# Optimization experiments

Measured on AMD Instinct MI355X. Metric: run time of the kernel, lower is better.

## Reference

```python
import jax, jax.numpy as jnp
import numpy as np

N, E = 50000, 800000
IN_D, HID_D, OUT_D = 128, 64, 64
EPS_BN = 1e-5
NEG_SLOPE = 0.2


def _xavier(key, shape):
    fan_in, fan_out = shape[0], shape[-1]
    lim = float(np.sqrt(6.0 / (fan_in + fan_out)))
    return jax.random.uniform(key, shape, jnp.float32, -lim, lim)


def setup_inputs() -> dict:
    key = jax.random.key(0)
    ks = jax.random.split(key, 10)
    x = jax.random.normal(ks[0], (N, IN_D), jnp.float32)
    edge_index = jax.random.randint(ks[1], (2, E), 0, N, jnp.int64)
    return {
        "x": x,
        "edge_index": edge_index,
        "W1": _xavier(ks[2], (IN_D, HID_D)),
        "att_src1": _xavier(ks[3], (1, HID_D))[0],
        "att_dst1": _xavier(ks[4], (1, HID_D))[0],
        "bias1": jnp.zeros((HID_D,), jnp.float32),
        "gamma": jnp.ones((HID_D,), jnp.float32),
        "beta": jnp.zeros((HID_D,), jnp.float32),
        "W2": _xavier(ks[5], (HID_D, OUT_D)),
        "att_src2": _xavier(ks[6], (1, OUT_D))[0],
        "att_dst2": _xavier(ks[7], (1, OUT_D))[0],
        "bias2": jnp.zeros((OUT_D,), jnp.float32),
    }


def _gat_conv(x, src, dst, W, a_src, a_dst, bias, n_nodes):
    # h: [N, D_out]; messages flow src -> dst; softmax over edges per dst node
    h = x @ W
    alpha_s = h @ a_src  # [N]
    alpha_d = h @ a_dst  # [N]
    e = jax.nn.leaky_relu(alpha_s[src] + alpha_d[dst], NEG_SLOPE)  # [E]
    e_max = jax.ops.segment_max(e, dst, num_segments=n_nodes)
    e = jnp.exp(e - e_max[dst])
    denom = jax.ops.segment_sum(e, dst, num_segments=n_nodes)
    alpha = e / (denom[dst] + 1e-16)  # [E]
    out = jax.ops.segment_sum(h[src] * alpha[:, None], dst, num_segments=n_nodes)
    return out + bias


def _batchnorm(x, gamma, beta):
    mu = jnp.mean(x, axis=0)
    var = jnp.var(x, axis=0)
    return (x - mu) * jax.lax.rsqrt(var + EPS_BN) * gamma + beta


def reference(x, edge_index, W1, att_src1, att_dst1, bias1, gamma, beta,
              W2, att_src2, att_dst2, bias2):
    n_nodes = x.shape[0]
    loops = jnp.arange(n_nodes, dtype=edge_index.dtype)
    src = jnp.concatenate([edge_index[0], loops])  # add self loops (PyG default)
    dst = jnp.concatenate([edge_index[1], loops])
    h = _gat_conv(x, src, dst, W1, att_src1, att_dst1, bias1, n_nodes)
    h = jax.nn.relu(_batchnorm(h, gamma, beta))
    return _gat_conv(h, src, dst, W2, att_src2, att_dst2, bias2, n_nodes)
```

## Files before the change

### kernel.cpp

```cpp
#include <hip/hip_runtime.h>

#define N_NODES 50000
#define E_EDGES 800000
#define NE_TOT  (E_EDGES + N_NODES)
#define IND     128
#define HID     64
#define CAP_X   32
#define NEG_SLOPE 0.2f

typedef short v8s __attribute__((ext_vector_type(8)));
typedef float v4f __attribute__((ext_vector_type(4)));

#define SWZ(row, byte) ((byte) ^ (((row) & 7) << 4))

static __device__ __forceinline__ unsigned short f2bf(float f) {
    unsigned u = __float_as_uint(f);
    return (unsigned short)((u + 0x7FFF + ((u >> 16) & 1)) >> 16);
}
static __device__ __forceinline__ float bf2f(unsigned short u) {
    return __uint_as_float(((unsigned)u) << 16);
}

__global__ void k_init(const float* __restrict__ W1, const float* __restrict__ W2,
                       int* __restrict__ cnt, float* __restrict__ sums,
                       unsigned short* __restrict__ w1t, unsigned short* __restrict__ w2t) {
    int g = blockIdx.x * 256 + threadIdx.x;
    if (g < 8 * N_NODES) cnt[g] = 0;
    if (g < 128) sums[g] = 0.f;
    if (g < 64 * IND) { int c = g >> 7, k = g & 127; w1t[g] = f2bf(W1[k * 64 + c]); }
    if (g < 64 * 64)  { int c = g >> 6, k = g & 63;  w2t[g] = f2bf(W2[k * 64 + c]); }
}

__global__ void k_scatter(const int* __restrict__ ei, int* __restrict__ cnt,
                          unsigned short* __restrict__ bucket) {
    int xcc;
    asm("s_getreg_b32 %0, hwreg(20, 0, 32)" : "=s"(xcc));
    xcc &= 7;
    int e = blockIdx.x * 256 + threadIdx.x;
    if (e >= NE_TOT) return;
    int s, d;
    if (e < E_EDGES) { s = ei[e]; d = ei[E_EDGES + e]; }
    else { s = d = e - E_EDGES; }
    int pos = atomicAdd(&cnt[xcc * N_NODES + d], 1);
    if (pos < CAP_X) bucket[((size_t)(xcc * CAP_X + pos)) * N_NODES + d] = (unsigned short)s;
}

__global__ __launch_bounds__(256) void k_gemm1(
    const float* __restrict__ x, const unsigned short* __restrict__ w1t,
    const float* __restrict__ as_w, const float* __restrict__ ad_w,
    unsigned short* __restrict__ hbf, float* __restrict__ as_out, float* __restrict__ ad_out)
{
    __shared__ __align__(16) char sA[64 * 256];
    __shared__ __align__(16) char sB[64 * 256];
    __shared__ float sAs[64], sAd[64];
    int tid = threadIdx.x;
    int row0 = blockIdx.x * 64;

#pragma unroll
    for (int i = 0; i < 8; ++i) {
        int idx = i * 256 + tid;
        int r = idx >> 5, c4 = idx & 31;
        int gr = row0 + r; if (gr >= N_NODES) gr = N_NODES - 1;
        float4 v = ((const float4*)(x + (size_t)gr * IND))[c4];
        ushort4 b; b.x = f2bf(v.x); b.y = f2bf(v.y); b.z = f2bf(v.z); b.w = f2bf(v.w);
        *(ushort4*)(sA + r * 256 + SWZ(r, c4 * 8)) = b;
    }
#pragma unroll
    for (int i = 0; i < 4; ++i) {
        int idx = i * 256 + tid;
        int r = idx >> 4, c8 = idx & 15;
        v8s wv = *(const v8s*)(w1t + idx * 8);
        *(v8s*)(sB + r * 256 + SWZ(r, c8 * 16)) = wv;
    }
    if (tid < 64) { sAs[tid] = as_w[tid]; sAd[tid] = ad_w[tid]; }
    __syncthreads();

    int w = tid >> 6, lane = tid & 63;
    int arow = w * 16 + (lane & 15);
    int kb   = (lane >> 4) * 16;
    v4f acc[4] = {};
#pragma unroll
    for (int ks = 0; ks < 4; ++ks) {
        v8s a = *(const v8s*)(sA + arow * 256 + SWZ(arow, ks * 64 + kb));
#pragma unroll
        for (int ct = 0; ct < 4; ++ct) {
            int brow = ct * 16 + (lane & 15);
            v8s b = *(const v8s*)(sB + brow * 256 + SWZ(brow, ks * 64 + kb));
            acc[ct] = __builtin_amdgcn_mfma_f32_16x16x32_bf16(a, b, acc[ct], 0, 0, 0);
        }
    }

    int cbase = lane & 15;
    int rloc  = (lane >> 4) * 4;
#pragma unroll
    for (int ct = 0; ct < 4; ++ct)
#pragma unroll
        for (int rg = 0; rg < 4; ++rg) {
            int row = row0 + w * 16 + rloc + rg;
            if (row < N_NODES) hbf[(size_t)row * 64 + ct * 16 + cbase] = f2bf(acc[ct][rg]);
        }
#pragma unroll
    for (int rg = 0; rg < 4; ++rg) {
        float vs = 0.f, vd = 0.f;
#pragma unroll
        for (int ct = 0; ct < 4; ++ct) {
            vs = fmaf(acc[ct][rg], sAs[ct * 16 + cbase], vs);
            vd = fmaf(acc[ct][rg], sAd[ct * 16 + cbase], vd);
        }
        vs += __shfl_xor(vs, 1, 64); vd += __shfl_xor(vd, 1, 64);
        vs += __shfl_xor(vs, 2, 64); vd += __shfl_xor(vd, 2, 64);
        vs += __shfl_xor(vs, 4, 64); vd += __shfl_xor(vd, 4, 64);
        vs += __shfl_xor(vs, 8, 64); vd += __shfl_xor(vd, 8, 64);
        int row = row0 + w * 16 + rloc + rg;
        if (cbase == 0 && row < N_NODES) { as_out[row] = vs; ad_out[row] = vd; }
    }
}

template <bool OUT_BF16>
__global__ __launch_bounds__(256) void k_agg(
    const unsigned short* __restrict__ hin, const float* __restrict__ as_, const float* __restrict__ ad_,
    const int* __restrict__ cnt, const unsigned short* __restrict__ bucket,
    const float* __restrict__ bias, void* __restrict__ outv)
{
    int wave = threadIdx.x >> 6, lane = threadIdx.x & 63;
    int n = blockIdx.x * 4 + wave;
    if (n >= N_NODES) return;

    int pref[9]; pref[0] = 0;
#pragma unroll
    for (int xx = 0; xx < 8; ++xx)
        pref[xx + 1] = pref[xx] + min(cnt[xx * N_NODES + n], CAP_X);
    int deg = min(pref[8], 64);

    int xseg = 0, base = 0;
#pragma unroll
    for (int i = 0; i < 7; ++i)
        if (lane >= pref[i + 1]) { xseg = i + 1; base = pref[i + 1]; }

    float adn = ad_[n];
    int s_l = 0;
    float e = -1e30f;
    if (lane < deg) {
        s_l = (int)bucket[((size_t)(xseg * CAP_X + (lane - base))) * N_NODES + n];
        float t = as_[s_l] + adn;
        e = t > 0.f ? t : NEG_SLOPE * t;
    }
    float m = e;
    for (int off = 32; off; off >>= 1) m = fmaxf(m, __shfl_xor(m, off, 64));
    float w_l = (lane < deg) ? __expf(e - m) : 0.f;
    float denom = w_l;
    for (int off = 32; off; off >>= 1) denom += __shfl_xor(denom, off, 64);

    float acc = 0.f;
    for (int t = 0; t < deg; t += 8) {
        int s0 = __shfl(s_l, t + 0), s1 = __shfl(s_l, t + 1);
        int s2 = __shfl(s_l, t + 2), s3 = __shfl(s_l, t + 3);
        int s4 = __shfl(s_l, t + 4), s5 = __shfl(s_l, t + 5);
        int s6 = __shfl(s_l, t + 6), s7 = __shfl(s_l, t + 7);
        float w0 = __shfl(w_l, t + 0), w1 = __shfl(w_l, t + 1);
        float w2 = __shfl(w_l, t + 2), w3 = __shfl(w_l, t + 3);
        float w4 = __shfl(w_l, t + 4), w5 = __shfl(w_l, t + 5);
        float w6 = __shfl(w_l, t + 6), w7 = __shfl(w_l, t + 7);
        float v0 = bf2f(hin[(size_t)s0 * HID + lane]);
        float v1 = bf2f(hin[(size_t)s1 * HID + lane]);
        float v2 = bf2f(hin[(size_t)s2 * HID + lane]);
        float v3 = bf2f(hin[(size_t)s3 * HID + lane]);
        float v4 = bf2f(hin[(size_t)s4 * HID + lane]);
        float v5 = bf2f(hin[(size_t)s5 * HID + lane]);
        float v6 = bf2f(hin[(size_t)s6 * HID + lane]);
        float v7 = bf2f(hin[(size_t)s7 * HID + lane]);
        acc = fmaf(w0, v0, acc); acc = fmaf(w1, v1, acc);
        acc = fmaf(w2, v2, acc); acc = fmaf(w3, v3, acc);
        acc = fmaf(w4, v4, acc); acc = fmaf(w5, v5, acc);
        acc = fmaf(w6, v6, acc); acc = fmaf(w7, v7, acc);
    }
    float inv = 1.f / (denom + 1e-16f);
    float res = acc * inv + bias[lane];
    if (OUT_BF16) ((unsigned short*)outv)[(size_t)n * HID + lane] = f2bf(res);
    else          ((float*)outv)[(size_t)n * HID + lane] = res;
}

__global__ __launch_bounds__(256) void k_bnstats(const unsigned short* __restrict__ h,
                                                 float* __restrict__ sums) {
    int lane = threadIdx.x & 63, wave = threadIdx.x >> 6;
    float s = 0.f, ss = 0.f;
    for (int r = blockIdx.x * 4 + wave; r < N_NODES; r += gridDim.x * 4) {
        float v = bf2f(h[(size_t)r * HID + lane]);
        s += v; ss = fmaf(v, v, ss);
    }
    __shared__ float ls[4][64], lss[4][64];
    ls[wave][lane] = s; lss[wave][lane] = ss;
    __syncthreads();
    if (wave == 0) {
        s  = ls[0][lane] + ls[1][lane] + ls[2][lane] + ls[3][lane];
        ss = lss[0][lane] + lss[1][lane] + lss[2][lane] + lss[3][lane];
        atomicAdd(&sums[lane], s);
        atomicAdd(&sums[64 + lane], ss);
    }
}

__global__ void k_bnfinal(const float* __restrict__ sums, const float* __restrict__ gamma,
                          const float* __restrict__ beta, float* __restrict__ ss_out) {
    int j = threadIdx.x;
    if (j >= 64) return;
    float mean = sums[j] * (1.f / N_NODES);
    float var  = sums[64 + j] * (1.f / N_NODES) - mean * mean;
    float sc = gamma[j] * rsqrtf(var + 1e-5f);
    ss_out[j] = sc;
    ss_out[64 + j] = beta[j] - mean * sc;
}

__global__ __launch_bounds__(256) void k_gemm2(
    const unsigned short* __restrict__ hin, const unsigned short* __restrict__ w2t,
    const float* __restrict__ ss,
    const float* __restrict__ as_w, const float* __restrict__ ad_w,
    unsigned short* __restrict__ h2bf, float* __restrict__ as_out, float* __restrict__ ad_out)
{
    __shared__ __align__(16) char sA[64 * 128];
    __shared__ __align__(16) char sB[64 * 128];
    __shared__ float sAs[64], sAd[64];
    int tid = threadIdx.x;
    int row0 = blockIdx.x * 64;

#pragma unroll
    for (int i = 0; i < 2; ++i) {
        int idx = i * 256 + tid;
        int r = idx >> 3, c8 = idx & 7;
        int gr = row0 + r; if (gr >= N_NODES) gr = N_NODES - 1;
        v8s hv = *(const v8s*)(hin + (size_t)gr * 64 + c8 * 8);
        unsigned short o[8];
#pragma unroll
        for (int j = 0; j < 8; ++j) {
            float f = bf2f((unsigned short)hv[j]);
            float sc = ss[c8 * 8 + j], sh = ss[64 + c8 * 8 + j];
            o[j] = f2bf(fmaxf(fmaf(f, sc, sh), 0.f));
        }
        *(v8s*)(sA + r * 128 + SWZ(r, c8 * 16)) = *(v8s*)o;
    }
#pragma unroll
    for (int i = 0; i < 2; ++i) {
        int idx = i * 256 + tid;
        int r = idx >> 3, c8 = idx & 7;
        v8s wv = *(const v8s*)(w2t + idx * 8);
        *(v8s*)(sB + r * 128 + SWZ(r, c8 * 16)) = wv;
    }
    if (tid < 64) { sAs[tid] = as_w[tid]; sAd[tid] = ad_w[tid]; }
    __syncthreads();

    int w = tid >> 6, lane = tid & 63;
    int arow = w * 16 + (lane & 15);
    int kb   = (lane >> 4) * 16;
    v4f acc[4] = {};
#pragma unroll
    for (int ks = 0; ks < 2; ++ks) {
        v8s a = *(const v8s*)(sA + arow * 128 + SWZ(arow, ks * 64 + kb));
#pragma unroll
        for (int ct = 0; ct < 4; ++ct) {
            int brow = ct * 16 + (lane & 15);
            v8s b = *(const v8s*)(sB + brow * 128 + SWZ(brow, ks * 64 + kb));
            acc[ct] = __builtin_amdgcn_mfma_f32_16x16x32_bf16(a, b, acc[ct], 0, 0, 0);
        }
    }

    int cbase = lane & 15;
    int rloc  = (lane >> 4) * 4;
#pragma unroll
    for (int ct = 0; ct < 4; ++ct)
#pragma unroll
        for (int rg = 0; rg < 4; ++rg) {
            int row = row0 + w * 16 + rloc + rg;
            if (row < N_NODES) h2bf[(size_t)row * 64 + ct * 16 + cbase] = f2bf(acc[ct][rg]);
        }
#pragma unroll
    for (int rg = 0; rg < 4; ++rg) {
        float vs = 0.f, vd = 0.f;
#pragma unroll
        for (int ct = 0; ct < 4; ++ct) {
            vs = fmaf(acc[ct][rg], sAs[ct * 16 + cbase], vs);
            vd = fmaf(acc[ct][rg], sAd[ct * 16 + cbase], vd);
        }
        vs += __shfl_xor(vs, 1, 64); vd += __shfl_xor(vd, 1, 64);
        vs += __shfl_xor(vs, 2, 64); vd += __shfl_xor(vd, 2, 64);
        vs += __shfl_xor(vs, 4, 64); vd += __shfl_xor(vd, 4, 64);
        vs += __shfl_xor(vs, 8, 64); vd += __shfl_xor(vd, 8, 64);
        int row = row0 + w * 16 + rloc + rg;
        if (cbase == 0 && row < N_NODES) { as_out[row] = vs; ad_out[row] = vd; }
    }
}

extern "C" void kernel_launch(void* const* d_in, const int* in_sizes, int n_in,
                              void* d_out, int out_size, void* d_ws, size_t ws_size,
                              hipStream_t stream) {
    const float* x        = (const float*)d_in[0];
    const int*   ei       = (const int*)d_in[1];
    const float* W1       = (const float*)d_in[2];
    const float* att_src1 = (const float*)d_in[3];
    const float* att_dst1 = (const float*)d_in[4];
    const float* bias1    = (const float*)d_in[5];
    const float* gamma    = (const float*)d_in[6];
    const float* beta     = (const float*)d_in[7];
    const float* W2       = (const float*)d_in[8];
    const float* att_src2 = (const float*)d_in[9];
    const float* att_dst2 = (const float*)d_in[10];
    const float* bias2    = (const float*)d_in[11];
    float* out = (float*)d_out;

    char* ws = (char*)d_ws;
    size_t off = 0;
    auto alloc = [&](size_t bytes) { void* p = ws + off; off = (off + bytes + 255) & ~(size_t)255; return p; };
    unsigned short* h1     = (unsigned short*)alloc((size_t)N_NODES * HID * 2);
    float* as1    = (float*)alloc((size_t)N_NODES * 4);
    float* ad1    = (float*)alloc((size_t)N_NODES * 4);
    unsigned short* h1agg  = (unsigned short*)alloc((size_t)N_NODES * HID * 2);
    unsigned short* h2     = (unsigned short*)alloc((size_t)N_NODES * HID * 2);
    float* as2    = (float*)alloc((size_t)N_NODES * 4);
    float* ad2    = (float*)alloc((size_t)N_NODES * 4);
    int*   cnt    = (int*)alloc((size_t)8 * N_NODES * 4);
    unsigned short* bucket = (unsigned short*)alloc((size_t)8 * CAP_X * N_NODES * 2);
    float* sums   = (float*)alloc(128 * 4);
    float* bn_ss  = (float*)alloc(128 * 4);
    unsigned short* w1t = (unsigned short*)alloc(64 * IND * 2);
    unsigned short* w2t = (unsigned short*)alloc(64 * 64 * 2);

    int gemmBlocks = (N_NODES + 63) / 64;
    int edgeBlocks = (NE_TOT + 255) / 256;
    int initBlocks = (8 * N_NODES + 255) / 256;
    k_init<<<initBlocks, 256, 0, stream>>>(W1, W2, cnt, sums, w1t, w2t);
    k_gemm1<<<gemmBlocks, 256, 0, stream>>>(x, w1t, att_src1, att_dst1, h1, as1, ad1);
    k_scatter<<<edgeBlocks, 256, 0, stream>>>(ei, cnt, bucket);
    k_agg<true><<<(N_NODES + 3) / 4, 256, 0, stream>>>(h1, as1, ad1, cnt, bucket, bias1, h1agg);
    k_bnstats<<<256, 256, 0, stream>>>(h1agg, sums);
    k_bnfinal<<<1, 64, 0, stream>>>(sums, gamma, beta, bn_ss);
    k_gemm2<<<gemmBlocks, 256, 0, stream>>>(h1agg, w2t, bn_ss, att_src2, att_dst2, h2, as2, ad2);
    k_agg<false><<<(N_NODES + 3) / 4, 256, 0, stream>>>(h2, as2, ad2, cnt, bucket, bias2, out);
}
```

Measured before the change: 145.1 us.

## Fuse scatter into gemm1, fold BN finalize into gemm2, vectorize aggregation gathers

The edge-bucketing scatter now runs as extra blocks of the first GEMM kernel, and the BN scale/shift computation moves into gemm2's prologue, which removes two kernel launches. The aggregation loop now has each lane load a 4-element bf16 vector from one of 4 neighbours per step and combines the groups with cross-lane shuffles. This issues fewer, wider gather loads per neighbour row. The cost is the extra reduction shuffles, only 16 lanes storing results, and the scatter blocks sharing the GEMM kernel's LDS allocation, which may lower their occupancy.

```diff
diff --git a/kernel.cpp b/kernel.cpp
--- a/kernel.cpp
+++ b/kernel.cpp
@@ -7,6 +7,8 @@
 #define HID     64
 #define CAP_X   32
 #define NEG_SLOPE 0.2f
+#define GEMM_BLKS ((N_NODES + 63) / 64)
+#define EDGE_BLKS ((NE_TOT + 255) / 256)
 
 typedef short v8s __attribute__((ext_vector_type(8)));
 typedef float v4f __attribute__((ext_vector_type(4)));
@@ -31,31 +33,32 @@
     if (g < 64 * 64)  { int c = g >> 6, k = g & 63;  w2t[g] = f2bf(W2[k * 64 + c]); }
 }
 
-__global__ void k_scatter(const int* __restrict__ ei, int* __restrict__ cnt,
-                          unsigned short* __restrict__ bucket) {
-    int xcc;
-    asm("s_getreg_b32 %0, hwreg(20, 0, 32)" : "=s"(xcc));
-    xcc &= 7;
-    int e = blockIdx.x * 256 + threadIdx.x;
-    if (e >= NE_TOT) return;
-    int s, d;
-    if (e < E_EDGES) { s = ei[e]; d = ei[E_EDGES + e]; }
-    else { s = d = e - E_EDGES; }
-    int pos = atomicAdd(&cnt[xcc * N_NODES + d], 1);
-    if (pos < CAP_X) bucket[((size_t)(xcc * CAP_X + pos)) * N_NODES + d] = (unsigned short)s;
-}
-
-__global__ __launch_bounds__(256) void k_gemm1(
+__global__ __launch_bounds__(256) void k_fused1(
     const float* __restrict__ x, const unsigned short* __restrict__ w1t,
     const float* __restrict__ as_w, const float* __restrict__ ad_w,
-    unsigned short* __restrict__ hbf, float* __restrict__ as_out, float* __restrict__ ad_out)
+    unsigned short* __restrict__ hbf, float* __restrict__ as_out, float* __restrict__ ad_out,
+    const int* __restrict__ ei, int* __restrict__ cnt, unsigned short* __restrict__ bucket)
 {
     __shared__ __align__(16) char sA[64 * 256];
     __shared__ __align__(16) char sB[64 * 256];
     __shared__ float sAs[64], sAd[64];
     int tid = threadIdx.x;
+
+    if (blockIdx.x >= GEMM_BLKS) {
+        int xcc;
+        asm("s_getreg_b32 %0, hwreg(20, 0, 32)" : "=s"(xcc));
+        xcc &= 7;
+        int e = (blockIdx.x - GEMM_BLKS) * 256 + tid;
+        if (e >= NE_TOT) return;
+        int s, d;
+        if (e < E_EDGES) { s = ei[e]; d = ei[E_EDGES + e]; }
+        else { s = d = e - E_EDGES; }
+        int pos = atomicAdd(&cnt[xcc * N_NODES + d], 1);
+        if (pos < CAP_X) bucket[((size_t)(xcc * CAP_X + pos)) * N_NODES + d] = (unsigned short)s;
+        return;
+    }
+
     int row0 = blockIdx.x * 64;
-
 #pragma unroll
     for (int i = 0; i < 8; ++i) {
         int idx = i * 256 + tid;
@@ -151,33 +154,39 @@
     float denom = w_l;
     for (int off = 32; off; off >>= 1) denom += __shfl_xor(denom, off, 64);
 
-    float acc = 0.f;
+    int g = lane >> 4, fb = (lane & 15) * 4;
+    float a0 = 0.f, a1 = 0.f, a2 = 0.f, a3 = 0.f;
     for (int t = 0; t < deg; t += 8) {
-        int s0 = __shfl(s_l, t + 0), s1 = __shfl(s_l, t + 1);
-        int s2 = __shfl(s_l, t + 2), s3 = __shfl(s_l, t + 3);
-        int s4 = __shfl(s_l, t + 4), s5 = __shfl(s_l, t + 5);
-        int s6 = __shfl(s_l, t + 6), s7 = __shfl(s_l, t + 7);
-        float w0 = __shfl(w_l, t + 0), w1 = __shfl(w_l, t + 1);
-        float w2 = __shfl(w_l, t + 2), w3 = __shfl(w_l, t + 3);
-        float w4 = __shfl(w_l, t + 4), w5 = __shfl(w_l, t + 5);
-        float w6 = __shfl(w_l, t + 6), w7 = __shfl(w_l, t + 7);
-        float v0 = bf2f(hin[(size_t)s0 * HID + lane]);
-        float v1 = bf2f(hin[(size_t)s1 * HID + lane]);
-        float v2 = bf2f(hin[(size_t)s2 * HID + lane]);
-        float v3 = bf2f(hin[(size_t)s3 * HID + lane]);
-        float v4 = bf2f(hin[(size_t)s4 * HID + lane]);
-        float v5 = bf2f(hin[(size_t)s5 * HID + lane]);
-        float v6 = bf2f(hin[(size_t)s6 * HID + lane]);
-        float v7 = bf2f(hin[(size_t)s7 * HID + lane]);
-        acc = fmaf(w0, v0, acc); acc = fmaf(w1, v1, acc);
-        acc = fmaf(w2, v2, acc); acc = fmaf(w3, v3, acc);
-        acc = fmaf(w4, v4, acc); acc = fmaf(w5, v5, acc);
-        acc = fmaf(w6, v6, acc); acc = fmaf(w7, v7, acc);
-    }
-    float inv = 1.f / (denom + 1e-16f);
-    float res = acc * inv + bias[lane];
-    if (OUT_BF16) ((unsigned short*)outv)[(size_t)n * HID + lane] = f2bf(res);
-    else          ((float*)outv)[(size_t)n * HID + lane] = res;
+        int sa = __shfl(s_l, t + g);
+        int sb = __shfl(s_l, t + 4 + g);
+        float wa = __shfl(w_l, t + g);
+        float wb = __shfl(w_l, t + 4 + g);
+        ushort4 ha = {0, 0, 0, 0}, hb = {0, 0, 0, 0};
+        if (t + g < deg)     ha = *(const ushort4*)(hin + (size_t)sa * HID + fb);
+        if (t + 4 + g < deg) hb = *(const ushort4*)(hin + (size_t)sb * HID + fb);
+        a0 = fmaf(wa, bf2f(ha.x), a0); a1 = fmaf(wa, bf2f(ha.y), a1);
+        a2 = fmaf(wa, bf2f(ha.z), a2); a3 = fmaf(wa, bf2f(ha.w), a3);
+        a0 = fmaf(wb, bf2f(hb.x), a0); a1 = fmaf(wb, bf2f(hb.y), a1);
+        a2 = fmaf(wb, bf2f(hb.z), a2); a3 = fmaf(wb, bf2f(hb.w), a3);
+    }
+    a0 += __shfl_xor(a0, 16, 64); a0 += __shfl_xor(a0, 32, 64);
+    a1 += __shfl_xor(a1, 16, 64); a1 += __shfl_xor(a1, 32, 64);
+    a2 += __shfl_xor(a2, 16, 64); a2 += __shfl_xor(a2, 32, 64);
+    a3 += __shfl_xor(a3, 16, 64); a3 += __shfl_xor(a3, 32, 64);
+
+    if (lane < 16) {
+        float inv = 1.f / (denom + 1e-16f);
+        float4 b4 = ((const float4*)bias)[lane];
+        float r0 = fmaf(a0, inv, b4.x), r1 = fmaf(a1, inv, b4.y);
+        float r2 = fmaf(a2, inv, b4.z), r3 = fmaf(a3, inv, b4.w);
+        if (OUT_BF16) {
+            ushort4 o; o.x = f2bf(r0); o.y = f2bf(r1); o.z = f2bf(r2); o.w = f2bf(r3);
+            *(ushort4*)((unsigned short*)outv + (size_t)n * HID + lane * 4) = o;
+        } else {
+            float4 o = {r0, r1, r2, r3};
+            *(float4*)((float*)outv + (size_t)n * HID + lane * 4) = o;
+        }
+    }
 }
 
 __global__ __launch_bounds__(256) void k_bnstats(const unsigned short* __restrict__ h,
@@ -199,28 +208,27 @@
     }
 }
 
-__global__ void k_bnfinal(const float* __restrict__ sums, const float* __restrict__ gamma,
-                          const float* __restrict__ beta, float* __restrict__ ss_out) {
-    int j = threadIdx.x;
-    if (j >= 64) return;
-    float mean = sums[j] * (1.f / N_NODES);
-    float var  = sums[64 + j] * (1.f / N_NODES) - mean * mean;
-    float sc = gamma[j] * rsqrtf(var + 1e-5f);
-    ss_out[j] = sc;
-    ss_out[64 + j] = beta[j] - mean * sc;
-}
-
 __global__ __launch_bounds__(256) void k_gemm2(
     const unsigned short* __restrict__ hin, const unsigned short* __restrict__ w2t,
-    const float* __restrict__ ss,
+    const float* __restrict__ sums, const float* __restrict__ gamma, const float* __restrict__ beta,
     const float* __restrict__ as_w, const float* __restrict__ ad_w,
     unsigned short* __restrict__ h2bf, float* __restrict__ as_out, float* __restrict__ ad_out)
 {
     __shared__ __align__(16) char sA[64 * 128];
     __shared__ __align__(16) char sB[64 * 128];
-    __shared__ float sAs[64], sAd[64];
+    __shared__ float sAs[64], sAd[64], sScale[64], sShift[64];
     int tid = threadIdx.x;
     int row0 = blockIdx.x * 64;
+
+    if (tid < 64) {
+        float mean = sums[tid] * (1.f / N_NODES);
+        float var  = sums[64 + tid] * (1.f / N_NODES) - mean * mean;
+        float sc = gamma[tid] * rsqrtf(var + 1e-5f);
+        sScale[tid] = sc;
+        sShift[tid] = beta[tid] - mean * sc;
+        sAs[tid] = as_w[tid]; sAd[tid] = ad_w[tid];
+    }
+    __syncthreads();
 
 #pragma unroll
     for (int i = 0; i < 2; ++i) {
@@ -232,8 +240,7 @@
 #pragma unroll
         for (int j = 0; j < 8; ++j) {
             float f = bf2f((unsigned short)hv[j]);
-            float sc = ss[c8 * 8 + j], sh = ss[64 + c8 * 8 + j];
-            o[j] = f2bf(fmaxf(fmaf(f, sc, sh), 0.f));
+            o[j] = f2bf(fmaxf(fmaf(f, sScale[c8 * 8 + j], sShift[c8 * 8 + j]), 0.f));
         }
         *(v8s*)(sA + r * 128 + SWZ(r, c8 * 16)) = *(v8s*)o;
     }
@@ -244,7 +251,6 @@
         v8s wv = *(const v8s*)(w2t + idx * 8);
         *(v8s*)(sB + r * 128 + SWZ(r, c8 * 16)) = wv;
     }
-    if (tid < 64) { sAs[tid] = as_w[tid]; sAd[tid] = ad_w[tid]; }
     __syncthreads();
 
     int w = tid >> 6, lane = tid & 63;
@@ -318,19 +324,16 @@
     int*   cnt    = (int*)alloc((size_t)8 * N_NODES * 4);
     unsigned short* bucket = (unsigned short*)alloc((size_t)8 * CAP_X * N_NODES * 2);
     float* sums   = (float*)alloc(128 * 4);
-    float* bn_ss  = (float*)alloc(128 * 4);
     unsigned short* w1t = (unsigned short*)alloc(64 * IND * 2);
     unsigned short* w2t = (unsigned short*)alloc(64 * 64 * 2);
 
-    int gemmBlocks = (N_NODES + 63) / 64;
-    int edgeBlocks = (NE_TOT + 255) / 256;
     int initBlocks = (8 * N_NODES + 255) / 256;
     k_init<<<initBlocks, 256, 0, stream>>>(W1, W2, cnt, sums, w1t, w2t);
-    k_gemm1<<<gemmBlocks, 256, 0, stream>>>(x, w1t, att_src1, att_dst1, h1, as1, ad1);
-    k_scatter<<<edgeBlocks, 256, 0, stream>>>(ei, cnt, bucket);
+    k_fused1<<<GEMM_BLKS + EDGE_BLKS, 256, 0, stream>>>(x, w1t, att_src1, att_dst1,
+                                                        h1, as1, ad1, ei, cnt, bucket);
     k_agg<true><<<(N_NODES + 3) / 4, 256, 0, stream>>>(h1, as1, ad1, cnt, bucket, bias1, h1agg);
     k_bnstats<<<256, 256, 0, stream>>>(h1agg, sums);
-    k_bnfinal<<<1, 64, 0, stream>>>(sums, gamma, beta, bn_ss);
-    k_gemm2<<<gemmBlocks, 256, 0, stream>>>(h1agg, w2t, bn_ss, att_src2, att_dst2, h2, as2, ad2);
+    k_gemm2<<<GEMM_BLKS, 256, 0, stream>>>(h1agg, w2t, sums, gamma, beta,
+                                           att_src2, att_dst2, h2, as2, ad2);
     k_agg<false><<<(N_NODES + 3) / 4, 256, 0, stream>>>(h2, as2, ad2, cnt, bucket, bias2, out);
 }
```

After: 137.4 us. 1.06x faster.
